# Performance work log

Measured on AMD Instinct MI355X. Metric: run time of the kernel, lower is better.

## Reference

```python
import jax, jax.numpy as jnp
import numpy as np

D = 512   # dim (number of groups)
H = 8192  # h = dim * v
U = 64    # u
V = H // D  # 16
N = 4096  # batch
EPS = 1e-12  # torch F.normalize eps


def setup_inputs() -> dict:
    key = jax.random.key(0)
    k_x, k_w1, k_b1, k_w2, k_b2 = jax.random.split(key, 5)
    x = jax.random.normal(k_x, (N, H), dtype=jnp.float32)
    # grouped Conv1d(dim*v, dim*u, k=1, groups=dim) == per-group [u, v] matmul
    s1 = 1.0 / np.sqrt(V)
    W1 = jax.random.uniform(k_w1, (D, U, V), jnp.float32, -s1, s1)
    b1 = jax.random.uniform(k_b1, (D, U), jnp.float32, -s1, s1)
    # grouped Conv1d(dim*u, dim, k=1, groups=dim) == per-group [1, u] matmul
    s2 = 1.0 / np.sqrt(U)
    W2 = jax.random.uniform(k_w2, (D, U), jnp.float32, -s2, s2)
    b2 = jax.random.uniform(k_b2, (D,), jnp.float32, -s2, s2)
    return {"x": x, "W1": W1, "b1": b1, "W2": W2, "b2": b2}


def reference(x, W1, b1, W2, b2):
    # x: [N, H] -> [N, D, V] (channel layout of Conv1d groups)
    xg = x.reshape(-1, D, V)
    # grouped 1x1 conv #1: per-group v -> u matmul, + bias
    h1 = jnp.einsum('ndv,duv->ndu', xg, W1) + b1  # [N, D, U]
    h1 = jax.nn.elu(h1)
    # grouped 1x1 conv #2: per-group u -> 1 matmul, + bias
    y = jnp.einsum('ndu,du->nd', h1, W2) + b2  # [N, D]
    # L2 normalize (torch F.normalize semantics: x / max(||x||, eps))
    nrm = jnp.sqrt(jnp.sum(y * y, axis=-1, keepdims=True))
    return y / jnp.maximum(nrm, EPS)
```

## Files before the change

### kernel.cpp

```cpp
#include <hip/hip_runtime.h>
#include <math.h>

#define D_ 512
#define H_ 8192
#define U_ 64
#define V_ 16
#define N_ 4096
#define DUV (D_ * U_ * V_)

#define BR 64
#define BG 8
#define XSTR (BG * V_ + 4)
#define YSTR 12

typedef __bf16 bf16x8 __attribute__((ext_vector_type(8)));
typedef __bf16 bf16x4 __attribute__((ext_vector_type(4)));
typedef float f32x4 __attribute__((ext_vector_type(4)));

__global__ __launch_bounds__(256) void k0_split_w1(const float* __restrict__ W1,
                                                   __bf16* __restrict__ wh) {
    __bf16* wl = wh + DUV;
    const int i4 = (blockIdx.x * 256 + threadIdx.x) * 4;
    f32x4 w = *(const f32x4*)(W1 + i4);
    bf16x4 h, l;
    #pragma unroll
    for (int j = 0; j < 4; ++j) {
        float wf = w[j];
        __bf16 hh = (__bf16)wf;
        h[j] = hh;
        l[j] = (__bf16)(wf - (float)hh);
    }
    *(bf16x4*)(wh + i4) = h;
    *(bf16x4*)(wl + i4) = l;
}

template <bool PRESPLIT>
__global__ __launch_bounds__(256, 4) void k1_div_encoder(
        const float* __restrict__ x,
        const float* __restrict__ W1,
        const __bf16* __restrict__ wsplit,
        const float* __restrict__ b1,
        const float* __restrict__ W2,
        const float* __restrict__ b2,
        float* __restrict__ y) {
    __shared__ float xs[BR][XSTR];
    __shared__ float ytile[BR][YSTR];

    const int tid  = threadIdx.x;
    const int lane = tid & 63;
    const int wave = __builtin_amdgcn_readfirstlane(tid >> 6);
    const int q    = lane >> 4;
    const int m    = lane & 15;
    const int vbase = (q & 1) * 8;

    const int nb = blockIdx.x & 63;
    const int db = blockIdx.x >> 6;
    const int r0 = nb * BR;
    const int d0 = db * BG;

    {
        const float* xg = x + (size_t)r0 * H_ + (size_t)d0 * V_;
        #pragma unroll
        for (int i = 0; i < 8; ++i) {
            const int flat = tid + i * 256;
            const int row  = flat >> 5;
            const int c4   = flat & 31;
            f32x4 v = *(const f32x4*)(xg + (size_t)row * H_ + c4 * 4);
            *(f32x4*)&xs[row][c4 * 4] = v;
        }
    }
    __syncthreads();

    #pragma unroll 1
    for (int gi = 0; gi < 2; ++gi) {
        const int gl = wave * 2 + gi;
        const int d  = d0 + gl;

        bf16x8 Afrag[4];
        if (PRESPLIT) {
            const __bf16* base = wsplit + (size_t)(q >> 1) * DUV;
            #pragma unroll
            for (int c = 0; c < 4; ++c) {
                Afrag[c] = *(const bf16x8*)(base +
                    ((size_t)d * U_ + c * 16 + m) * V_ + vbase);
            }
        } else {
            #pragma unroll
            for (int c = 0; c < 4; ++c) {
                const float* wp = W1 + ((size_t)d * U_ + c * 16 + m) * V_ + vbase;
                f32x4 w0 = *(const f32x4*)wp;
                f32x4 w1v = *(const f32x4*)(wp + 4);
                float wf[8] = {w0.x, w0.y, w0.z, w0.w, w1v.x, w1v.y, w1v.z, w1v.w};
                bf16x8 a;
                #pragma unroll
                for (int i = 0; i < 8; ++i) {
                    __bf16 h = (__bf16)wf[i];
                    __bf16 l = (__bf16)(wf[i] - (float)h);
                    a[i] = (q < 2) ? h : l;
                }
                Afrag[c] = a;
            }
        }

        f32x4 b1frag[4], w2frag[4];
        #pragma unroll
        for (int c = 0; c < 4; ++c) {
            b1frag[c] = *(const f32x4*)(b1 + (size_t)d * U_ + c * 16 + q * 4);
            w2frag[c] = *(const f32x4*)(W2 + (size_t)d * U_ + c * 16 + q * 4);
        }
        const float b2s = b2[d];

        #pragma unroll 2
        for (int t = 0; t < 4; ++t) {
            const float* bp = &xs[t * 16 + m][gl * V_ + vbase];
            f32x4 x0 = *(const f32x4*)bp;
            f32x4 x1 = *(const f32x4*)(bp + 4);
            float xf[8] = {x0.x, x0.y, x0.z, x0.w, x1.x, x1.y, x1.z, x1.w};
            bf16x8 bhi, blo;
            #pragma unroll
            for (int i = 0; i < 8; ++i) {
                __bf16 h = (__bf16)xf[i];
                bhi[i] = h;
                blo[i] = (__bf16)(xf[i] - (float)h);
            }

            float partial = 0.0f;
            #pragma unroll
            for (int c = 0; c < 4; ++c) {
                f32x4 acc = b1frag[c];
                acc = __builtin_amdgcn_mfma_f32_16x16x32_bf16(Afrag[c], bhi, acc, 0, 0, 0);
                acc = __builtin_amdgcn_mfma_f32_16x16x32_bf16(Afrag[c], blo, acc, 0, 0, 0);
                #pragma unroll
                for (int r = 0; r < 4; ++r) {
                    float h = acc[r];
                    float e = fmaxf(h, __expf(fminf(h, 0.0f)) - 1.0f);
                    partial = fmaf(w2frag[c][r], e, partial);
                }
            }
            partial += __shfl_xor(partial, 16, 64);
            partial += __shfl_xor(partial, 32, 64);
            if (q == 0) {
                ytile[t * 16 + m][gl] = partial + b2s;
            }
        }
    }
    __syncthreads();

    if (tid < 128) {
        const int row  = tid >> 1;
        const int half = tid & 1;
        f32x4 v = *(const f32x4*)&ytile[row][half * 4];
        *(f32x4*)(y + (size_t)(r0 + row) * D_ + d0 + half * 4) = v;
    }
}

__global__ __launch_bounds__(256) void k2_l2_normalize(float* __restrict__ y) {
    const int n = blockIdx.x;
    const int t = threadIdx.x;
    float* row = y + (size_t)n * D_;

    float v0 = row[t];
    float v1 = row[t + 256];
    float ss = v0 * v0 + v1 * v1;

    #pragma unroll
    for (int off = 32; off > 0; off >>= 1) {
        ss += __shfl_down(ss, off, 64);
    }

    __shared__ float wsum[4];
    if ((t & 63) == 0) wsum[t >> 6] = ss;
    __syncthreads();
    const float tot = wsum[0] + wsum[1] + wsum[2] + wsum[3];

    const float scale = 1.0f / fmaxf(sqrtf(tot), 1e-12f);

    row[t]       = v0 * scale;
    row[t + 256] = v1 * scale;
}

extern "C" void kernel_launch(void* const* d_in, const int* in_sizes, int n_in,
                              void* d_out, int out_size, void* d_ws, size_t ws_size,
                              hipStream_t stream) {
    const float* x  = (const float*)d_in[0];
    const float* W1 = (const float*)d_in[1];
    const float* b1 = (const float*)d_in[2];
    const float* W2 = (const float*)d_in[3];
    const float* b2 = (const float*)d_in[4];
    float* y = (float*)d_out;

    const dim3 grid((N_ / BR) * (D_ / BG));
    if (ws_size >= (size_t)(2 * DUV * sizeof(__bf16))) {
        __bf16* wh = (__bf16*)d_ws;
        k0_split_w1<<<dim3(DUV / 4 / 256), dim3(256), 0, stream>>>(W1, wh);
        k1_div_encoder<true><<<grid, dim3(256), 0, stream>>>(
            x, W1, wh, b1, W2, b2, y);
    } else {
        k1_div_encoder<false><<<grid, dim3(256), 0, stream>>>(
            x, W1, (const __bf16*)nullptr, b1, W2, b2, y);
    }
    k2_l2_normalize<<<dim3(N_), dim3(256), 0, stream>>>(y);
}
```

Baseline: 220.6 us.

## Pre-split x into bf16 hi/lo in LDS, fold log2e scaling, atomic reduce

x is now split into bf16 hi/lo halves once while staging into shared memory, so each MFMA tile no longer redoes the conversion. W1 and b1 are prescaled by log2(e) and W2 by ln2, which lets the ELU use exp2 directly without a multiply. The cross-lane shuffle reduction is replaced by LDS atomicAdd into a zeroed y tile, with b2 added at the final store. This adds an extra small preprocessing kernel and LDS atomic contention, and the prescaling slightly perturbs rounding.

Measured after the change: 231.1 us. 1.05x slower.

```diff
diff --git a/kernel.cpp b/kernel.cpp
--- a/kernel.cpp
+++ b/kernel.cpp
@@ -7,15 +7,21 @@
 #define V_ 16
 #define N_ 4096
 #define DUV (D_ * U_ * V_)
+#define DU  (D_ * U_)
+
+#define LOG2E 1.4426950408889634f
+#define LN2   0.6931471805599453f
 
 #define BR 64
 #define BG 8
-#define XSTR (BG * V_ + 4)
+#define XSTR 136
 #define YSTR 12
 
 typedef __bf16 bf16x8 __attribute__((ext_vector_type(8)));
 typedef __bf16 bf16x4 __attribute__((ext_vector_type(4)));
 typedef float f32x4 __attribute__((ext_vector_type(4)));
+
+#define WS_NEEDED (2 * DUV * sizeof(__bf16) + 2 * DU * sizeof(float))
 
 __global__ __launch_bounds__(256) void k0_split_w1(const float* __restrict__ W1,
                                                    __bf16* __restrict__ wh) {
@@ -25,13 +31,26 @@
     bf16x4 h, l;
     #pragma unroll
     for (int j = 0; j < 4; ++j) {
-        float wf = w[j];
+        float wf = w[j] * LOG2E;
         __bf16 hh = (__bf16)wf;
         h[j] = hh;
         l[j] = (__bf16)(wf - (float)hh);
     }
     *(bf16x4*)(wh + i4) = h;
     *(bf16x4*)(wl + i4) = l;
+}
+
+__global__ __launch_bounds__(256) void k0_scale_b1w2(const float* __restrict__ b1,
+                                                     const float* __restrict__ W2,
+                                                     float* __restrict__ b1s,
+                                                     float* __restrict__ w2s) {
+    const int i4 = (blockIdx.x * 256 + threadIdx.x) * 4;
+    f32x4 b = *(const f32x4*)(b1 + i4);
+    f32x4 w = *(const f32x4*)(W2 + i4);
+    #pragma unroll
+    for (int j = 0; j < 4; ++j) { b[j] *= LOG2E; w[j] *= LN2; }
+    *(f32x4*)(b1s + i4) = b;
+    *(f32x4*)(w2s + i4) = w;
 }
 
 template <bool PRESPLIT>
@@ -43,15 +62,16 @@
         const float* __restrict__ W2,
         const float* __restrict__ b2,
         float* __restrict__ y) {
-    __shared__ float xs[BR][XSTR];
-    __shared__ float ytile[BR][YSTR];
+    __shared__ __bf16 xhi[BR][XSTR];
+    __shared__ __bf16 xlo[BR][XSTR];
+    __shared__ float  ytile[BR][YSTR];
 
     const int tid  = threadIdx.x;
     const int lane = tid & 63;
     const int wave = __builtin_amdgcn_readfirstlane(tid >> 6);
     const int q    = lane >> 4;
     const int m    = lane & 15;
-    const int vbase = (q & 1) * 8;
+    const int vhalf = (q & 1) * 8;
 
     const int nb = blockIdx.x & 63;
     const int db = blockIdx.x >> 6;
@@ -66,7 +86,19 @@
             const int row  = flat >> 5;
             const int c4   = flat & 31;
             f32x4 v = *(const f32x4*)(xg + (size_t)row * H_ + c4 * 4);
-            *(f32x4*)&xs[row][c4 * 4] = v;
+            bf16x4 h, l;
+            #pragma unroll
+            for (int j = 0; j < 4; ++j) {
+                __bf16 hh = (__bf16)v[j];
+                h[j] = hh;
+                l[j] = (__bf16)(v[j] - (float)hh);
+            }
+            *(bf16x4*)&xhi[row][c4 * 4] = h;
+            *(bf16x4*)&xlo[row][c4 * 4] = l;
+        }
+        #pragma unroll
+        for (int k = tid; k < BR * YSTR; k += 256) {
+            ((float*)ytile)[k] = 0.0f;
         }
     }
     __syncthreads();
@@ -77,52 +109,45 @@
         const int d  = d0 + gl;
 
         bf16x8 Afrag[4];
+        f32x4 b1frag[4], w2frag[4];
         if (PRESPLIT) {
             const __bf16* base = wsplit + (size_t)(q >> 1) * DUV;
             #pragma unroll
             for (int c = 0; c < 4; ++c) {
                 Afrag[c] = *(const bf16x8*)(base +
-                    ((size_t)d * U_ + c * 16 + m) * V_ + vbase);
+                    ((size_t)d * U_ + c * 16 + m) * V_ + vhalf);
+                b1frag[c] = *(const f32x4*)(b1 + (size_t)d * U_ + c * 16 + q * 4);
+                w2frag[c] = *(const f32x4*)(W2 + (size_t)d * U_ + c * 16 + q * 4);
             }
         } else {
             #pragma unroll
             for (int c = 0; c < 4; ++c) {
-                const float* wp = W1 + ((size_t)d * U_ + c * 16 + m) * V_ + vbase;
+                const float* wp = W1 + ((size_t)d * U_ + c * 16 + m) * V_ + vhalf;
                 f32x4 w0 = *(const f32x4*)wp;
                 f32x4 w1v = *(const f32x4*)(wp + 4);
                 float wf[8] = {w0.x, w0.y, w0.z, w0.w, w1v.x, w1v.y, w1v.z, w1v.w};
                 bf16x8 a;
                 #pragma unroll
                 for (int i = 0; i < 8; ++i) {
-                    __bf16 h = (__bf16)wf[i];
-                    __bf16 l = (__bf16)(wf[i] - (float)h);
-                    a[i] = (q < 2) ? h : l;
+                    float ws_ = wf[i] * LOG2E;
+                    __bf16 h = (__bf16)ws_;
+                    __bf16 lo = (__bf16)(ws_ - (float)h);
+                    a[i] = (q < 2) ? h : lo;
                 }
                 Afrag[c] = a;
-            }
-        }
-
-        f32x4 b1frag[4], w2frag[4];
-        #pragma unroll
-        for (int c = 0; c < 4; ++c) {
-            b1frag[c] = *(const f32x4*)(b1 + (size_t)d * U_ + c * 16 + q * 4);
-            w2frag[c] = *(const f32x4*)(W2 + (size_t)d * U_ + c * 16 + q * 4);
-        }
-        const float b2s = b2[d];
+                f32x4 bb = *(const f32x4*)(b1 + (size_t)d * U_ + c * 16 + q * 4);
+                f32x4 ww = *(const f32x4*)(W2 + (size_t)d * U_ + c * 16 + q * 4);
+                #pragma unroll
+                for (int j = 0; j < 4; ++j) { bb[j] *= LOG2E; ww[j] *= LN2; }
+                b1frag[c] = bb;
+                w2frag[c] = ww;
+            }
+        }
 
         #pragma unroll 2
         for (int t = 0; t < 4; ++t) {
-            const float* bp = &xs[t * 16 + m][gl * V_ + vbase];
-            f32x4 x0 = *(const f32x4*)bp;
-            f32x4 x1 = *(const f32x4*)(bp + 4);
-            float xf[8] = {x0.x, x0.y, x0.z, x0.w, x1.x, x1.y, x1.z, x1.w};
-            bf16x8 bhi, blo;
-            #pragma unroll
-            for (int i = 0; i < 8; ++i) {
-                __bf16 h = (__bf16)xf[i];
-                bhi[i] = h;
-                blo[i] = (__bf16)(xf[i] - (float)h);
-            }
+            bf16x8 bhi = *(const bf16x8*)&xhi[t * 16 + m][gl * V_ + vhalf];
+            bf16x8 blo = *(const bf16x8*)&xlo[t * 16 + m][gl * V_ + vhalf];
 
             float partial = 0.0f;
             #pragma unroll
@@ -132,16 +157,15 @@
                 acc = __builtin_amdgcn_mfma_f32_16x16x32_bf16(Afrag[c], blo, acc, 0, 0, 0);
                 #pragma unroll
                 for (int r = 0; r < 4; ++r) {
-                    float h = acc[r];
-                    float e = fmaxf(h, __expf(fminf(h, 0.0f)) - 1.0f);
-                    partial = fmaf(w2frag[c][r], e, partial);
+                    float hp = acc[r];
+                    float mn = fminf(hp, 0.0f);
+                    float t2 = __builtin_amdgcn_exp2f(mn);
+                    float e  = fmaf(t2, LOG2E, -LOG2E);
+                    float vv = fmaxf(hp, e);
+                    partial  = fmaf(w2frag[c][r], vv, partial);
                 }
             }
-            partial += __shfl_xor(partial, 16, 64);
-            partial += __shfl_xor(partial, 32, 64);
-            if (q == 0) {
-                ytile[t * 16 + m][gl] = partial + b2s;
-            }
+            atomicAdd(&ytile[t * 16 + m][gl], partial);
         }
     }
     __syncthreads();
@@ -149,7 +173,10 @@
     if (tid < 128) {
         const int row  = tid >> 1;
         const int half = tid & 1;
-        f32x4 v = *(const f32x4*)&ytile[row][half * 4];
+        f32x4 v  = *(const f32x4*)&ytile[row][half * 4];
+        f32x4 bb = *(const f32x4*)(b2 + d0 + half * 4);
+        #pragma unroll
+        for (int j = 0; j < 4; ++j) v[j] += bb[j];
         *(f32x4*)(y + (size_t)(r0 + row) * D_ + d0 + half * 4) = v;
     }
 }
@@ -190,11 +217,14 @@
     float* y = (float*)d_out;
 
     const dim3 grid((N_ / BR) * (D_ / BG));
-    if (ws_size >= (size_t)(2 * DUV * sizeof(__bf16))) {
-        __bf16* wh = (__bf16*)d_ws;
+    if (ws_size >= WS_NEEDED) {
+        __bf16* wh  = (__bf16*)d_ws;
+        float* b1s  = (float*)((char*)d_ws + 2 * DUV * sizeof(__bf16));
+        float* w2s  = b1s + DU;
         k0_split_w1<<<dim3(DUV / 4 / 256), dim3(256), 0, stream>>>(W1, wh);
+        k0_scale_b1w2<<<dim3(DU / 4 / 256), dim3(256), 0, stream>>>(b1, W2, b1s, w2s);
         k1_div_encoder<true><<<grid, dim3(256), 0, stream>>>(
-            x, W1, wh, b1, W2, b2, y);
+            x, W1, wh, b1s, w2s, b2, y);
     } else {
         k1_div_encoder<false><<<grid, dim3(256), 0, stream>>>(
             x, W1, (const __bf16*)nullptr, b1, W2, b2, y);
```
